# Kernel optimization log

Measured on AMD Instinct MI355X. Metric: run time of the kernel, lower is better.

Reference implementation:

```python
import jax, jax.numpy as jnp
import numpy as np

N_NODES = 50000
N_EDGES = 800000
N_PRED = 100000  # pos and neg each
D_IN = 256
D_HID = 128  # hard-coded hidden width of conv1
D_OUT = 128  # out_channels


def _lin_params(key, fan_in, fan_out, dtype=jnp.float32):
    kw, kb = jax.random.split(key)
    s = 1.0 / np.sqrt(fan_in)
    W = jax.random.uniform(kw, (fan_in, fan_out), dtype, -s, s)
    b = jax.random.uniform(kb, (fan_out,), dtype, -s, s)
    return W, b


def setup_inputs() -> dict:
    key = jax.random.key(0)
    ks = jax.random.split(key, 16)
    inp = {
        "x": jax.random.normal(ks[0], (N_NODES, D_IN), jnp.float32),
        "edge_index": jax.random.randint(ks[1], (2, N_EDGES), 0, N_NODES, jnp.int64),
        "pos_edge_index": jax.random.randint(ks[2], (2, N_PRED), 0, N_NODES, jnp.int64),
        "neg_edge_index": jax.random.randint(ks[3], (2, N_PRED), 0, N_NODES, jnp.int64),
    }
    # conv1: TransformerConv(D_IN -> D_HID), heads=1, root_weight=True
    inp["Wq1"], inp["bq1"] = _lin_params(ks[4], D_IN, D_HID)
    inp["Wk1"], inp["bk1"] = _lin_params(ks[5], D_IN, D_HID)
    inp["Wv1"], inp["bv1"] = _lin_params(ks[6], D_IN, D_HID)
    inp["Ws1"], inp["bs1"] = _lin_params(ks[7], D_IN, D_HID)
    # conv2: TransformerConv(D_HID -> D_OUT)
    inp["Wq2"], inp["bq2"] = _lin_params(ks[8], D_HID, D_OUT)
    inp["Wk2"], inp["bk2"] = _lin_params(ks[9], D_HID, D_OUT)
    inp["Wv2"], inp["bv2"] = _lin_params(ks[10], D_HID, D_OUT)
    inp["Ws2"], inp["bs2"] = _lin_params(ks[11], D_HID, D_OUT)
    # final edge scorer Linear(D_OUT, 1)
    inp["Wl"], inp["bl"] = _lin_params(ks[12], D_OUT, 1)
    return inp


def _transformer_conv(x, Wq, bq, Wk, bk, Wv, bv, Ws, bs, src, dst, n_nodes):
    # PyG TransformerConv, heads=1, concat=True, root_weight=True, no edge attrs.
    C = Wq.shape[1]
    q = x @ Wq + bq  # [N, C] queries (destination side)
    k = x @ Wk + bk  # [N, C] keys (source side)
    v = x @ Wv + bv  # [N, C] values (source side)
    # per-edge attention logits, softmax normalized over incoming edges of dst
    alpha = jnp.einsum("ec,ec->e", q[dst], k[src]) / jnp.sqrt(jnp.asarray(C, x.dtype))
    amax = jax.lax.stop_gradient(jax.ops.segment_max(alpha, dst, num_segments=n_nodes))
    ex = jnp.exp(alpha - amax[dst])
    den = jax.ops.segment_sum(ex, dst, num_segments=n_nodes)
    w = ex / den[dst]  # [E]
    agg = jax.ops.segment_sum(v[src] * w[:, None], dst, num_segments=n_nodes)  # [N, C]
    return agg + (x @ Ws + bs)  # skip connection (lin_skip)


def reference(x, edge_index, pos_edge_index, neg_edge_index,
              Wq1, bq1, Wk1, bk1, Wv1, bv1, Ws1, bs1,
              Wq2, bq2, Wk2, bk2, Wv2, bv2, Ws2, bs2,
              Wl, bl):
    src, dst = edge_index[0], edge_index[1]
    h = _transformer_conv(x, Wq1, bq1, Wk1, bk1, Wv1, bv1, Ws1, bs1, src, dst, N_NODES)
    h = jax.nn.relu(h)
    h = _transformer_conv(h, Wq2, bq2, Wk2, bk2, Wv2, bv2, Ws2, bs2, src, dst, N_NODES)
    ei = jnp.concatenate([pos_edge_index, neg_edge_index], axis=-1)  # [2, 2*N_PRED]
    prod = h[ei[0]] * h[ei[1]]  # [2*N_PRED, D_OUT]
    return (prod @ Wl + bl).squeeze(-1)  # [2*N_PRED]
```

## Files before the change

### kernel.cpp

```cpp
#include <hip/hip_runtime.h>
#include <cstdint>
#include <cstddef>

#define NN 50000
#define NE 800000
#define NP 100000

#define EPB    3125
#define NBUK   196

#define CVT_BLOCKS   12500
#define PACKW_BLOCKS 1024
#define RADIX1_BLOCKS 256

typedef _Float16 h8v __attribute__((ext_vector_type(8)));
typedef _Float16 h4v __attribute__((ext_vector_type(4)));
typedef _Float16 h2v __attribute__((ext_vector_type(2)));
typedef float    f4v __attribute__((ext_vector_type(4)));

#define ATTN_SCALE 0.088388347648318447f

__device__ inline void load_lds16(const void* gptr, void* ldsptr) {
  __builtin_amdgcn_global_load_lds(
      (const __attribute__((address_space(1))) void*)gptr,
      (__attribute__((address_space(3))) void*)ldsptr, 16, 0, 0);
}

__device__ inline float dot8(h8v a, h8v b, float c) {
  union U { h8v v; h2v p[4]; };
  U ua; ua.v = a;
  U ub; ub.v = b;
#if __has_builtin(__builtin_amdgcn_fdot2)
  c = __builtin_amdgcn_fdot2(ua.p[0], ub.p[0], c, false);
  c = __builtin_amdgcn_fdot2(ua.p[1], ub.p[1], c, false);
  c = __builtin_amdgcn_fdot2(ua.p[2], ub.p[2], c, false);
  c = __builtin_amdgcn_fdot2(ua.p[3], ub.p[3], c, false);
#else
#pragma unroll
  for (int j = 0; j < 8; ++j) c = fmaf((float)a[j], (float)b[j], c);
#endif
  return c;
}

__global__ __launch_bounds__(256) void prep_kernel(
    const float* __restrict__ x, _Float16* __restrict__ Xf,
    const float* __restrict__ Wq1, const float* __restrict__ Wk1,
    const float* __restrict__ Wv1, const float* __restrict__ Ws1,
    const float* __restrict__ Wq2, const float* __restrict__ Wk2,
    const float* __restrict__ Wv2, const float* __restrict__ Ws2,
    _Float16* __restrict__ WT1, _Float16* __restrict__ WT2,
    const int* __restrict__ dst, unsigned short* __restrict__ erank,
    int* __restrict__ blockcount) {
  __shared__ int cnt[256];
  int b = blockIdx.x;
  int tid = threadIdx.x;
  if (b < CVT_BLOCKS) {
    int i = b * 256 + tid;
    float4 xv = ((const float4*)x)[i];
    h4v o = {(_Float16)xv.x, (_Float16)xv.y, (_Float16)xv.z, (_Float16)xv.w};
    ((h4v*)Xf)[i] = o;
  } else if (b < CVT_BLOCKS + PACKW_BLOCKS) {
    int bb = b - CVT_BLOCKS;
    if (bb < 512) {
      int n = bb;
      const float* W;
      switch (n >> 7) {
        case 0:  W = Wq1; break;
        case 1:  W = Wk1; break;
        case 2:  W = Wv1; break;
        default: W = Ws1; break;
      }
      WT1[(size_t)n * 256 + tid] = (_Float16)W[(size_t)tid * 128 + (n & 127)];
    } else if (tid < 128) {
      int n = bb - 512;
      const float* W;
      switch (n >> 7) {
        case 0:  W = Wq2; break;
        case 1:  W = Wk2; break;
        case 2:  W = Wv2; break;
        default: W = Ws2; break;
      }
      WT2[(size_t)n * 128 + tid] = (_Float16)W[(size_t)tid * 128 + (n & 127)];
    }
  } else {
    int blk = b - CVT_BLOCKS - PACKW_BLOCKS;
    cnt[tid] = 0;
    __syncthreads();
    int base = blk * EPB;
    for (int i = tid; i < EPB; i += 256) {
      int e = base + i;
      erank[e] = (unsigned short)atomicAdd(&cnt[dst[e] >> 8], 1);
    }
    __syncthreads();
    blockcount[tid * 256 + blk] = cnt[tid];
  }
}

__global__ __launch_bounds__(256) void scan1_kernel(const int* __restrict__ deg,
                                                    int* __restrict__ loc,
                                                    int* __restrict__ bsum, int n) {
  __shared__ int sh[256];
  int tid = threadIdx.x;
  int i = blockIdx.x * 256 + tid;
  int val = (i < n) ? deg[i] : 0;
  sh[tid] = val;
  __syncthreads();
  for (int off = 1; off < 256; off <<= 1) {
    int add = (tid >= off) ? sh[tid - off] : 0;
    __syncthreads();
    sh[tid] += add;
    __syncthreads();
  }
  if (i < n) loc[i] = sh[tid] - val;
  if (tid == 255) bsum[blockIdx.x] = sh[255];
}

__global__ __launch_bounds__(256) void scan23_kernel(const int* __restrict__ loc,
                                                     const int* __restrict__ bsum,
                                                     int* __restrict__ outv,
                                                     int n, int E) {
  __shared__ int sh[256];
  int bid = blockIdx.x, tid = threadIdx.x;
  int pre = 0;
  for (int j = tid; j < bid; j += 256) pre += bsum[j];
  sh[tid] = pre;
  __syncthreads();
  for (int off = 128; off > 0; off >>= 1) {
    if (tid < off) sh[tid] += sh[tid + off];
    __syncthreads();
  }
  int base = sh[0];
  int i = bid * 256 + tid;
  if (i < n) outv[i] = loc[i] + base;
  if (bid == 0 && tid == 0) outv[n] = E;
}

__global__ __launch_bounds__(256) void radix2_kernel(
    const int* __restrict__ src, const int* __restrict__ dst,
    const int* __restrict__ bcscan, const unsigned short* __restrict__ erank,
    unsigned* __restrict__ tmp) {
  int blk = blockIdx.x, tid = threadIdx.x;
  int base = blk * EPB;
  for (int i = tid; i < EPB; i += 256) {
    int e = base + i;
    int d = dst[e];
    int pos = bcscan[(d >> 8) * 256 + blk] + (int)erank[e];
    tmp[pos] = (unsigned)src[e] | ((unsigned)(d & 255) << 16);
  }
}

__global__ __launch_bounds__(256) void radix3_kernel(
    const unsigned* __restrict__ tmp, const int* __restrict__ bcscan,
    unsigned short* __restrict__ rank2,
    int* __restrict__ offs, unsigned short* __restrict__ csr_src) {
  __shared__ int cnt[256];
  __shared__ int sh[256];
  int tid = threadIdx.x, bu = blockIdx.x;
  cnt[tid] = 0;
  __syncthreads();
  int bstart = bcscan[bu * 256];
  int bend   = bcscan[(bu + 1) * 256];
  for (int i = bstart + tid; i < bend; i += 256) {
    unsigned u = tmp[i];
    rank2[i] = (unsigned short)atomicAdd(&cnt[u >> 16], 1);
  }
  __syncthreads();
  int v = cnt[tid];
  sh[tid] = v;
  __syncthreads();
  for (int off = 1; off < 256; off <<= 1) {
    int add = (tid >= off) ? sh[tid - off] : 0;
    __syncthreads();
    sh[tid] += add;
    __syncthreads();
  }
  int excl = sh[tid] - v;
  int node = bu * 256 + tid;
  if (node < NN) offs[node] = bstart + excl;
  if (bu == 0 && tid == 0) offs[NN] = NE;
  __syncthreads();
  cnt[tid] = excl;
  __syncthreads();
  for (int i = bstart + tid; i < bend; i += 256) {
    unsigned u = tmp[i];
    csr_src[bstart + cnt[u >> 16] + (int)rank2[i]] = (unsigned short)(u & 0xffffu);
  }
}

__global__ __launch_bounds__(256) void gemm_pb_kernel(
    const _Float16* __restrict__ A, int M, int K,
    const _Float16* __restrict__ BT,
    const float* __restrict__ bq, const float* __restrict__ bk,
    const float* __restrict__ bv, const float* __restrict__ bs,
    _Float16* __restrict__ Oq, _Float16* __restrict__ Okv,
    _Float16* __restrict__ Os) {
  extern __shared__ _Float16 smem[];
  _Float16* Bs = smem;
  _Float16* As = smem + 128 * K;

  const int tx = threadIdx.x;
  const int w = tx >> 6;
  const int lane = tx & 63;
  const int lr = lane & 15;
  const int q = lane >> 4;
  const int wm = w >> 1, wn = w & 1;
  const int p = blockIdx.y;
  const int rowshift = (K == 256) ? 5 : 4;
  const int rowchunks = K >> 3;

  {
    const _Float16* Bp = BT + (size_t)p * 128 * K;
    int total = 128 * rowchunks;
    for (int s0 = w * 64; s0 < total; s0 += 256) {
      int s = s0 + lane;
      int r = s >> rowshift;
      int sc = s & (rowchunks - 1);
      int g = (sc & ~7) | ((sc & 7) ^ (r & 7));
      load_lds16(Bp + (size_t)r * K + g * 8, &Bs[(size_t)s0 * 8]);
    }
  }

  const float* bp = (p == 0) ? bq : (p == 1) ? bk : (p == 2) ? bv : bs;

  for (int t = 0; t < 4; ++t) {
    int tile = t * 98 + blockIdx.x;
    int row0 = tile * 128;
    if (row0 >= M) break;

    f4v acc[4][4];
#pragma unroll
    for (int i = 0; i < 4; ++i)
#pragma unroll
      for (int j = 0; j < 4; ++j) acc[i][j] = (f4v){0.f, 0.f, 0.f, 0.f};

    for (int k0 = 0; k0 < K; k0 += 64) {
      __syncthreads();
#pragma unroll
      for (int o = 0; o < 4; ++o) {
        int i = o * 4 + w;
        int r = i * 8 + (lane >> 3);
        int cl = (lane & 7) ^ (r & 7);
        int gr = row0 + r;
        if (gr > M - 1) gr = M - 1;
        load_lds16(A + (size_t)gr * K + k0 + cl * 8, &As[i * 8 * 64]);
      }
      __syncthreads();

#pragma unroll
      for (int kk = 0; kk < 2; ++kk) {
        h8v af[4], bf[4];
#pragma unroll
        for (int tt = 0; tt < 4; ++tt) {
          int row = wm * 64 + tt * 16 + lr;
          af[tt] = *(const h8v*)&As[row * 64 + (((kk * 4 + q) ^ (row & 7)) * 8)];
          int col = wn * 64 + tt * 16 + lr;
          int ck = (k0 >> 3) + kk * 4 + q;
          int swz = (ck & ~7) | ((ck & 7) ^ (col & 7));
          bf[tt] = *(const h8v*)&Bs[(size_t)col * K + swz * 8];
        }
#pragma unroll
        for (int mt = 0; mt < 4; ++mt)
#pragma unroll
          for (int nt = 0; nt < 4; ++nt)
            acc[mt][nt] = __builtin_amdgcn_mfma_f32_16x16x32_f16(af[mt], bf[nt],
                                                                 acc[mt][nt], 0, 0, 0);
      }
    }

#pragma unroll
    for (int half = 0; half < 2; ++half) {
      __syncthreads();
      if (wm == half) {
#pragma unroll
        for (int nt = 0; nt < 4; ++nt) {
          int col = wn * 64 + nt * 16 + lr;
          float bval = bp[col];
#pragma unroll
          for (int mt = 0; mt < 4; ++mt)
#pragma unroll
            for (int reg = 0; reg < 4; ++reg) {
              int r = mt * 16 + q * 4 + reg;
              As[r * 128 + col] = (_Float16)(acc[mt][nt][reg] + bval);
            }
        }
      }
      __syncthreads();
#pragma unroll
      for (int i = 0; i < 4; ++i) {
        int sl = i * 256 + tx;
        int rr = sl >> 4;
        int col = (sl & 15) * 8;
        int grow = row0 + half * 64 + rr;
        if (grow < M) {
          _Float16* dstp;
          switch (p) {
            case 0:  dstp = Oq  + (size_t)grow * 128 + col;       break;
            case 1:  dstp = Okv + (size_t)grow * 256 + col;       break;
            case 2:  dstp = Okv + (size_t)grow * 256 + 128 + col; break;
            default: dstp = Os  + (size_t)grow * 128 + col;       break;
          }
          *(h8v*)dstp = *(const h8v*)&As[rr * 128 + col];
        }
      }
    }
  }
}

__global__ __launch_bounds__(256) void attn_fused_kernel(
    const _Float16* __restrict__ qf, const _Float16* __restrict__ kvf,
    const _Float16* __restrict__ sf,
    const int* __restrict__ offs, const unsigned short* __restrict__ csr_src,
    _Float16* __restrict__ hf, int n_nodes, int do_relu) {
  int node = (int)((blockIdx.x * 256u + threadIdx.x) >> 6);
  if (node >= n_nodes) return;
  int lane = threadIdx.x & 63;
  int g = lane >> 4;
  int t = lane & 15;

  h8v qv = *(const h8v*)(qf + (size_t)node * 128 + t * 8);
  int beg = offs[node], end = offs[node + 1];

  float den = 0.f;
  float acc[8];
#pragma unroll
  for (int j = 0; j < 8; ++j) acc[j] = 0.f;

  int e = beg + g;
  int sn0 = 0, sn1 = 0;
  if (e < end) sn0 = csr_src[e];
  if (e + 4 < end) sn1 = csr_src[e + 4];

  for (; e + 4 < end; e += 8) {
    const _Float16* r0 = kvf + (size_t)sn0 * 256 + t * 8;
    const _Float16* r1 = kvf + (size_t)sn1 * 256 + t * 8;
    h8v k0 = *(const h8v*)r0, v0 = *(const h8v*)(r0 + 128);
    h8v k1 = *(const h8v*)r1, v1 = *(const h8v*)(r1 + 128);
    int nn0 = (e + 8  < end) ? (int)csr_src[e + 8]  : 0;
    int nn1 = (e + 12 < end) ? (int)csr_src[e + 12] : 0;
    float p0 = dot8(qv, k0, 0.f);
    float p1 = dot8(qv, k1, 0.f);
    p0 += __shfl_xor(p0, 1); p1 += __shfl_xor(p1, 1);
    p0 += __shfl_xor(p0, 2); p1 += __shfl_xor(p1, 2);
    p0 += __shfl_xor(p0, 4); p1 += __shfl_xor(p1, 4);
    p0 += __shfl_xor(p0, 8); p1 += __shfl_xor(p1, 8);
    float w0 = __expf(p0 * ATTN_SCALE);
    float w1 = __expf(p1 * ATTN_SCALE);
    den += w0 + w1;
#pragma unroll
    for (int j = 0; j < 8; ++j) {
      acc[j] = fmaf(w0, (float)v0[j], acc[j]);
      acc[j] = fmaf(w1, (float)v1[j], acc[j]);
    }
    sn0 = nn0; sn1 = nn1;
  }
  if (e < end) {
    const _Float16* r0 = kvf + (size_t)sn0 * 256 + t * 8;
    h8v k0 = *(const h8v*)r0, v0 = *(const h8v*)(r0 + 128);
    float p0 = dot8(qv, k0, 0.f);
    p0 += __shfl_xor(p0, 1);
    p0 += __shfl_xor(p0, 2);
    p0 += __shfl_xor(p0, 4);
    p0 += __shfl_xor(p0, 8);
    float w0 = __expf(p0 * ATTN_SCALE);
    den += w0;
#pragma unroll
    for (int j = 0; j < 8; ++j) acc[j] = fmaf(w0, (float)v0[j], acc[j]);
  }

#pragma unroll
  for (int j = 0; j < 8; ++j) {
    acc[j] += __shfl_xor(acc[j], 16);
    acc[j] += __shfl_xor(acc[j], 32);
  }
  den += __shfl_xor(den, 16);
  den += __shfl_xor(den, 32);

  if (g == 0) {
    float inv = (end > beg) ? 1.f / den : 0.f;
    h8v sk = *(const h8v*)(sf + (size_t)node * 128 + t * 8);
    h8v of;
#pragma unroll
    for (int j = 0; j < 8; ++j) {
      float o = fmaf(acc[j], inv, (float)sk[j]);
      if (do_relu) o = fmaxf(o, 0.f);
      of[j] = (_Float16)o;
    }
    *(h8v*)(hf + (size_t)node * 128 + t * 8) = of;
  }
}

__global__ __launch_bounds__(256) void scorer_kernel(
    const _Float16* __restrict__ hf,
    const int* __restrict__ pos0, const int* __restrict__ pos1,
    const int* __restrict__ neg0, const int* __restrict__ neg1,
    const float* __restrict__ Wl, const float* __restrict__ bl,
    float* __restrict__ out, int npred) {
  int eid = (int)((blockIdx.x * 256u + threadIdx.x) >> 4);
  if (eid >= 2 * npred) return;
  int t = threadIdx.x & 15;

  int a, b;
  if (eid < npred) { a = pos0[eid]; b = pos1[eid]; }
  else             { a = neg0[eid - npred]; b = neg1[eid - npred]; }

  h8v ha = *(const h8v*)(hf + (size_t)a * 128 + t * 8);
  h8v hb = *(const h8v*)(hf + (size_t)b * 128 + t * 8);
  const float4* wp = (const float4*)(Wl + t * 8);
  float4 w0 = wp[0], w1 = wp[1];
  float wl[8] = {w0.x, w0.y, w0.z, w0.w, w1.x, w1.y, w1.z, w1.w};
  float p = 0.f;
#pragma unroll
  for (int j = 0; j < 8; ++j)
    p = fmaf((float)ha[j] * (float)hb[j], wl[j], p);
  p += __shfl_xor(p, 1);
  p += __shfl_xor(p, 2);
  p += __shfl_xor(p, 4);
  p += __shfl_xor(p, 8);
  if (t == 0) out[eid] = p + bl[0];
}

extern "C" void kernel_launch(void* const* d_in, const int* in_sizes, int n_in,
                              void* d_out, int out_size, void* d_ws, size_t ws_size,
                              hipStream_t stream) {
  const float* x   = (const float*)d_in[0];
  const int*   ei  = (const int*)d_in[1];
  const int*   pos = (const int*)d_in[2];
  const int*   neg = (const int*)d_in[3];
  const float* Wq1 = (const float*)d_in[4];  const float* bq1 = (const float*)d_in[5];
  const float* Wk1 = (const float*)d_in[6];  const float* bk1 = (const float*)d_in[7];
  const float* Wv1 = (const float*)d_in[8];  const float* bv1 = (const float*)d_in[9];
  const float* Ws1 = (const float*)d_in[10]; const float* bs1 = (const float*)d_in[11];
  const float* Wq2 = (const float*)d_in[12]; const float* bq2 = (const float*)d_in[13];
  const float* Wk2 = (const float*)d_in[14]; const float* bk2 = (const float*)d_in[15];
  const float* Wv2 = (const float*)d_in[16]; const float* bv2 = (const float*)d_in[17];
  const float* Ws2 = (const float*)d_in[18]; const float* bs2 = (const float*)d_in[19];
  const float* Wl  = (const float*)d_in[20]; const float* bl  = (const float*)d_in[21];
  float* out = (float*)d_out;

  const size_t NODE_C = (size_t)NN * 128;
  char* p = (char*)d_ws;
  _Float16* qf  = (_Float16*)p; p += NODE_C * 2;
  _Float16* kvf = (_Float16*)p; p += NODE_C * 4;
  _Float16* sf  = (_Float16*)p; p += NODE_C * 2;
  _Float16* h1  = (_Float16*)p; p += NODE_C * 2;
  _Float16* h2  = (_Float16*)p; p += NODE_C * 2;
  _Float16* Xf  = (_Float16*)p; p += (size_t)NN * 256 * 2;
  _Float16* WT1 = (_Float16*)p; p += 512 * 256 * 2;
  _Float16* WT2 = (_Float16*)p; p += 512 * 128 * 2;
  unsigned short* erank = (unsigned short*)p; p += (size_t)NE * 2;
  unsigned short* rank2 = (unsigned short*)p; p += (size_t)NE * 2;
  unsigned* tmp = (unsigned*)p;  p += (size_t)NE * 4;
  int* bc     = (int*)p;         p += 65536 * 4;
  int* bcloc  = (int*)p;         p += 65536 * 4;
  int* bcbs   = (int*)p;         p += 256 * 4;
  int* bcscan = (int*)p;         p += 65544 * 4;
  int* offs   = (int*)p;         p += (size_t)(NN + 8) * 4;
  unsigned short* csr_src = (unsigned short*)p; p += (size_t)NE * 2;

  const int* e_src = ei;
  const int* e_dst = ei + NE;

  prep_kernel<<<CVT_BLOCKS + PACKW_BLOCKS + RADIX1_BLOCKS, 256, 0, stream>>>(
      x, Xf, Wq1, Wk1, Wv1, Ws1, Wq2, Wk2, Wv2, Ws2, WT1, WT2,
      e_dst, erank, bc);

  scan1_kernel<<<256, 256, 0, stream>>>(bc, bcloc, bcbs, 65536);
  scan23_kernel<<<256, 256, 0, stream>>>(bcloc, bcbs, bcscan, 65536, NE);

  radix2_kernel<<<256, 256, 0, stream>>>(e_src, e_dst, bcscan, erank, tmp);
  radix3_kernel<<<NBUK, 256, 0, stream>>>(tmp, bcscan, rank2, offs, csr_src);

  dim3 ggrid(98, 4);
  int attn_blocks = (NN * 64 + 255) / 256;
  size_t lds1 = (size_t)128 * (256 + 64) * 2;
  size_t lds2 = (size_t)128 * (128 + 64) * 2;

  gemm_pb_kernel<<<ggrid, 256, lds1, stream>>>(Xf, NN, 256, WT1,
                                               bq1, bk1, bv1, bs1, qf, kvf, sf);
  attn_fused_kernel<<<attn_blocks, 256, 0, stream>>>(
      qf, kvf, sf, offs, csr_src, h1, NN, 1);

  gemm_pb_kernel<<<ggrid, 256, lds2, stream>>>(h1, NN, 128, WT2,
                                               bq2, bk2, bv2, bs2, qf, kvf, sf);
  attn_fused_kernel<<<attn_blocks, 256, 0, stream>>>(
      qf, kvf, sf, offs, csr_src, h2, NN, 0);

  scorer_kernel<<<(2 * NP * 16 + 255) / 256, 256, 0, stream>>>(
      h2, pos, pos + NP, neg, neg + NP, Wl, bl, out, NP);
}
```

Baseline: 350.7 us.

## Read GEMM weights from global/L2 and double-buffer A tiles

The projection GEMM no longer stages the full weight slice in LDS. It reads B fragments straight from global memory, relying on L2 and cache hits. The A tile is double-buffered in a static 32KB LDS array so the next k-step's load overlaps the current MFMA work. The persistent 98-block loop over four row tiles becomes one block per 128-row tile (391x4 grid), which cuts LDS per block and should raise occupancy. The risk is that uncoalesced per-lane global B loads sit in the MFMA inner loop, and there is only one barrier per k-step.

```diff
diff --git a/kernel.cpp b/kernel.cpp
--- a/kernel.cpp
+++ b/kernel.cpp
@@ -187,16 +187,14 @@
   }
 }
 
-__global__ __launch_bounds__(256) void gemm_pb_kernel(
+__global__ __launch_bounds__(256) void gemm_l2b_kernel(
     const _Float16* __restrict__ A, int M, int K,
     const _Float16* __restrict__ BT,
     const float* __restrict__ bq, const float* __restrict__ bk,
     const float* __restrict__ bv, const float* __restrict__ bs,
     _Float16* __restrict__ Oq, _Float16* __restrict__ Okv,
     _Float16* __restrict__ Os) {
-  extern __shared__ _Float16 smem[];
-  _Float16* Bs = smem;
-  _Float16* As = smem + 128 * K;
+  __shared__ _Float16 As[2][128 * 64];
 
   const int tx = threadIdx.x;
   const int w = tx >> 6;
@@ -205,102 +203,91 @@
   const int q = lane >> 4;
   const int wm = w >> 1, wn = w & 1;
   const int p = blockIdx.y;
-  const int rowshift = (K == 256) ? 5 : 4;
-  const int rowchunks = K >> 3;
-
-  {
-    const _Float16* Bp = BT + (size_t)p * 128 * K;
-    int total = 128 * rowchunks;
-    for (int s0 = w * 64; s0 < total; s0 += 256) {
-      int s = s0 + lane;
-      int r = s >> rowshift;
-      int sc = s & (rowchunks - 1);
-      int g = (sc & ~7) | ((sc & 7) ^ (r & 7));
-      load_lds16(Bp + (size_t)r * K + g * 8, &Bs[(size_t)s0 * 8]);
-    }
-  }
-
+  const int row0 = blockIdx.x * 128;
+
+  f4v acc[4][4];
+#pragma unroll
+  for (int i = 0; i < 4; ++i)
+#pragma unroll
+    for (int j = 0; j < 4; ++j) acc[i][j] = (f4v){0.f, 0.f, 0.f, 0.f};
+
+#define STAGE_A(buf, kbase)                                              \
+  {                                                                      \
+    _Pragma("unroll")                                                    \
+    for (int o = 0; o < 4; ++o) {                                        \
+      int i = o * 4 + w;                                                 \
+      int r = i * 8 + (lane >> 3);                                       \
+      int cl = (lane & 7) ^ (r & 7);                                     \
+      int gr = row0 + r;                                                 \
+      if (gr > M - 1) gr = M - 1;                                        \
+      load_lds16(A + (size_t)gr * K + (kbase) + cl * 8,                  \
+                 &As[buf][i * 8 * 64]);                                  \
+    }                                                                    \
+  }
+
+  STAGE_A(0, 0);
+  int cur = 0;
+
+  for (int k0 = 0; k0 < K; k0 += 64) {
+    __syncthreads();
+    if (k0 + 64 < K) STAGE_A(cur ^ 1, k0 + 64);
+
+#pragma unroll
+    for (int kk = 0; kk < 2; ++kk) {
+      h8v af[4], bf[4];
+#pragma unroll
+      for (int t = 0; t < 4; ++t) {
+        int row = wm * 64 + t * 16 + lr;
+        af[t] = *(const h8v*)&As[cur][row * 64 + (((kk * 4 + q) ^ (row & 7)) * 8)];
+        int col = p * 128 + wn * 64 + t * 16 + lr;
+        bf[t] = *(const h8v*)(BT + (size_t)col * K + k0 + kk * 32 + q * 8);
+      }
+#pragma unroll
+      for (int mt = 0; mt < 4; ++mt)
+#pragma unroll
+        for (int nt = 0; nt < 4; ++nt)
+          acc[mt][nt] = __builtin_amdgcn_mfma_f32_16x16x32_f16(af[mt], bf[nt],
+                                                               acc[mt][nt], 0, 0, 0);
+    }
+    cur ^= 1;
+  }
+#undef STAGE_A
+
+  _Float16* Ep = &As[0][0];
   const float* bp = (p == 0) ? bq : (p == 1) ? bk : (p == 2) ? bv : bs;
-
-  for (int t = 0; t < 4; ++t) {
-    int tile = t * 98 + blockIdx.x;
-    int row0 = tile * 128;
-    if (row0 >= M) break;
-
-    f4v acc[4][4];
-#pragma unroll
-    for (int i = 0; i < 4; ++i)
-#pragma unroll
-      for (int j = 0; j < 4; ++j) acc[i][j] = (f4v){0.f, 0.f, 0.f, 0.f};
-
-    for (int k0 = 0; k0 < K; k0 += 64) {
-      __syncthreads();
-#pragma unroll
-      for (int o = 0; o < 4; ++o) {
-        int i = o * 4 + w;
-        int r = i * 8 + (lane >> 3);
-        int cl = (lane & 7) ^ (r & 7);
-        int gr = row0 + r;
-        if (gr > M - 1) gr = M - 1;
-        load_lds16(A + (size_t)gr * K + k0 + cl * 8, &As[i * 8 * 64]);
+#pragma unroll
+  for (int half = 0; half < 2; ++half) {
+    __syncthreads();
+    if (wm == half) {
+#pragma unroll
+      for (int nt = 0; nt < 4; ++nt) {
+        int col = wn * 64 + nt * 16 + lr;
+        float bval = bp[col];
+#pragma unroll
+        for (int mt = 0; mt < 4; ++mt)
+#pragma unroll
+          for (int reg = 0; reg < 4; ++reg) {
+            int r = mt * 16 + q * 4 + reg;
+            Ep[r * 128 + col] = (_Float16)(acc[mt][nt][reg] + bval);
+          }
       }
-      __syncthreads();
-
-#pragma unroll
-      for (int kk = 0; kk < 2; ++kk) {
-        h8v af[4], bf[4];
-#pragma unroll
-        for (int tt = 0; tt < 4; ++tt) {
-          int row = wm * 64 + tt * 16 + lr;
-          af[tt] = *(const h8v*)&As[row * 64 + (((kk * 4 + q) ^ (row & 7)) * 8)];
-          int col = wn * 64 + tt * 16 + lr;
-          int ck = (k0 >> 3) + kk * 4 + q;
-          int swz = (ck & ~7) | ((ck & 7) ^ (col & 7));
-          bf[tt] = *(const h8v*)&Bs[(size_t)col * K + swz * 8];
+    }
+    __syncthreads();
+#pragma unroll
+    for (int i = 0; i < 4; ++i) {
+      int sl = i * 256 + tx;
+      int rr = sl >> 4;
+      int col = (sl & 15) * 8;
+      int grow = row0 + half * 64 + rr;
+      if (grow < M) {
+        _Float16* dstp;
+        switch (p) {
+          case 0:  dstp = Oq  + (size_t)grow * 128 + col;       break;
+          case 1:  dstp = Okv + (size_t)grow * 256 + col;       break;
+          case 2:  dstp = Okv + (size_t)grow * 256 + 128 + col; break;
+          default: dstp = Os  + (size_t)grow * 128 + col;       break;
         }
-#pragma unroll
-        for (int mt = 0; mt < 4; ++mt)
-#pragma unroll
-          for (int nt = 0; nt < 4; ++nt)
-            acc[mt][nt] = __builtin_amdgcn_mfma_f32_16x16x32_f16(af[mt], bf[nt],
-                                                                 acc[mt][nt], 0, 0, 0);
-      }
-    }
-
-#pragma unroll
-    for (int half = 0; half < 2; ++half) {
-      __syncthreads();
-      if (wm == half) {
-#pragma unroll
-        for (int nt = 0; nt < 4; ++nt) {
-          int col = wn * 64 + nt * 16 + lr;
-          float bval = bp[col];
-#pragma unroll
-          for (int mt = 0; mt < 4; ++mt)
-#pragma unroll
-            for (int reg = 0; reg < 4; ++reg) {
-              int r = mt * 16 + q * 4 + reg;
-              As[r * 128 + col] = (_Float16)(acc[mt][nt][reg] + bval);
-            }
-        }
-      }
-      __syncthreads();
-#pragma unroll
-      for (int i = 0; i < 4; ++i) {
-        int sl = i * 256 + tx;
-        int rr = sl >> 4;
-        int col = (sl & 15) * 8;
-        int grow = row0 + half * 64 + rr;
-        if (grow < M) {
-          _Float16* dstp;
-          switch (p) {
-            case 0:  dstp = Oq  + (size_t)grow * 128 + col;       break;
-            case 1:  dstp = Okv + (size_t)grow * 256 + col;       break;
-            case 2:  dstp = Okv + (size_t)grow * 256 + 128 + col; break;
-            default: dstp = Os  + (size_t)grow * 128 + col;       break;
-          }
-          *(h8v*)dstp = *(const h8v*)&As[rr * 128 + col];
-        }
+        *(h8v*)dstp = *(const h8v*)&Ep[rr * 128 + col];
       }
     }
   }
@@ -470,18 +457,16 @@
   radix2_kernel<<<256, 256, 0, stream>>>(e_src, e_dst, bcscan, erank, tmp);
   radix3_kernel<<<NBUK, 256, 0, stream>>>(tmp, bcscan, rank2, offs, csr_src);
 
-  dim3 ggrid(98, 4);
+  dim3 ggrid(391, 4);
   int attn_blocks = (NN * 64 + 255) / 256;
-  size_t lds1 = (size_t)128 * (256 + 64) * 2;
-  size_t lds2 = (size_t)128 * (128 + 64) * 2;
-
-  gemm_pb_kernel<<<ggrid, 256, lds1, stream>>>(Xf, NN, 256, WT1,
-                                               bq1, bk1, bv1, bs1, qf, kvf, sf);
+
+  gemm_l2b_kernel<<<ggrid, 256, 0, stream>>>(Xf, NN, 256, WT1,
+                                             bq1, bk1, bv1, bs1, qf, kvf, sf);
   attn_fused_kernel<<<attn_blocks, 256, 0, stream>>>(
       qf, kvf, sf, offs, csr_src, h1, NN, 1);
 
-  gemm_pb_kernel<<<ggrid, 256, lds2, stream>>>(h1, NN, 128, WT2,
-                                               bq2, bk2, bv2, bs2, qf, kvf, sf);
+  gemm_l2b_kernel<<<ggrid, 256, 0, stream>>>(h1, NN, 128, WT2,
+                                             bq2, bk2, bv2, bs2, qf, kvf, sf);
   attn_fused_kernel<<<attn_blocks, 256, 0, stream>>>(
       qf, kvf, sf, offs, csr_src, h2, NN, 0);
 
```

Measured after the change: 366.5 us. +4.5%, slower.
